# Performance work log

Hardware: AMD Instinct MI355X
Metric: run time of the kernel (lower is better)

The kernel has to match this reference:

```python
import jax, jax.numpy as jnp
import numpy as np

NH = 8  # n_heads
LN_EPS = 1e-5

def _ln(x, g, b):
    m = x.mean(-1, keepdims=True)
    v = ((x - m) ** 2).mean(-1, keepdims=True)
    return (x - m) / jnp.sqrt(v + LN_EPS) * g + b

def _l2norm(x):
    n = jnp.sqrt(jnp.sum(x * x, axis=-1, keepdims=True))
    return x / jnp.maximum(n, 1e-12)

def _block(h, inw, inb, outw, outb, g1, b1, g2, b2, w1, bb1, w2, bb2):
    B, T, D = h.shape
    hd = D // NH
    res = h
    hn = _ln(h, g1, b1)
    qkv = hn @ inw.T + inb
    q, k, v = jnp.split(qkv, 3, axis=-1)
    q = q.reshape(B, T, NH, hd)
    k = k.reshape(B, T, NH, hd)
    v = v.reshape(B, T, NH, hd)
    scores = jnp.einsum('bthd,bshd->bhts', q, k) / jnp.sqrt(jnp.asarray(hd, h.dtype))
    a = jax.nn.softmax(scores, axis=-1)
    o = jnp.einsum('bhts,bshd->bthd', a, v).reshape(B, T, D)
    h = res + o @ outw.T + outb
    f = _ln(h, g2, b2)
    f = jax.nn.gelu(f @ w1.T + bb1, approximate=False) @ w2.T + bb2
    return h + f

def setup_inputs() -> dict:
    B, T, IN, D, L, NS, NP = 8, 1024, 1024, 512, 4, 1024, 512
    key = jax.random.key(0)
    ks = jax.random.split(key, 24)
    gn = jax.random.normal
    u = jax.random.uniform(ks[1], (B, T, NS), dtype=jnp.float32, minval=1e-6, maxval=1.0 - 1e-6)
    gumbel = -jnp.log(-jnp.log(u))
    s = lambda fan: 1.0 / np.sqrt(fan)
    inp = {
        'x': gn(ks[0], (B, T, IN), dtype=jnp.float32),
        'gumbel': gumbel,
        'sym_w': gn(ks[2], (D, IN)) * s(IN),
        'sym_b': jnp.zeros((D,)),
        'codebook': gn(ks[3], (NS, D)) * 0.1,
        'pos_enc': gn(ks[4], (1, 2000, D)) * 0.02,
        'attn_in_w': gn(ks[5], (L, 3 * D, D)) * s(D),
        'attn_in_b': jnp.zeros((L, 3 * D)),
        'attn_out_w': gn(ks[6], (L, D, D)) * s(D),
        'attn_out_b': jnp.zeros((L, D)),
        'n1_g': jnp.ones((L, D)), 'n1_b': jnp.zeros((L, D)),
        'n2_g': jnp.ones((L, D)), 'n2_b': jnp.zeros((L, D)),
        'ffn_w1': gn(ks[7], (L, 4 * D, D)) * s(D),
        'ffn_b1': jnp.zeros((L, 4 * D)),
        'ffn_w2': gn(ks[8], (L, D, 4 * D)) * s(4 * D),
        'ffn_b2': jnp.zeros((L, D)),
        'q_w': gn(ks[9], (D, D)) * s(D),
        'q_b': jnp.zeros((D,)),
        'qln_g': jnp.ones((D,)), 'qln_b': jnp.zeros((D,)),
        'patterns': gn(ks[10], (NP, D)) * s(D),
        'epoch': 0,
        'total_epochs': 100,
    }
    return inp

def reference(x, gumbel, sym_w, sym_b, codebook, pos_enc,
              attn_in_w, attn_in_b, attn_out_w, attn_out_b,
              n1_g, n1_b, n2_g, n2_b, ffn_w1, ffn_b1, ffn_w2, ffn_b2,
              q_w, q_b, qln_g, qln_b, patterns, epoch, total_epochs):
    B, T, _ = x.shape
    # SymbolizationLayer (soft, gumbel-softmax with tau=0.5)
    hp = x @ sym_w.T + sym_b                               # [B,T,D]
    logits_s = _l2norm(hp) @ _l2norm(codebook).T / 0.5     # [B,T,NS]
    soft = jax.nn.softmax((logits_s + gumbel) / 0.5, axis=-1)
    h = soft @ codebook + pos_enc[:, :T, :]
    # transformer blocks
    for i in range(attn_in_w.shape[0]):
        h = _block(h, attn_in_w[i], attn_in_b[i], attn_out_w[i], attn_out_b[i],
                   n1_g[i], n1_b[i], n2_g[i], n2_b[i],
                   ffn_w1[i], ffn_b1[i], ffn_w2[i], ffn_b2[i])
    # VQPatternMatrix (eval mode: hard assignments, no EMA updates)
    Q = _l2norm(_ln(h @ q_w.T + q_b, qln_g, qln_b))
    temp = max(0.5, 1.0 - 0.5 * epoch / total_epochs)
    logits = Q @ _l2norm(patterns).T / temp                # [B,T,NP]
    hard_idx = jnp.argmax(logits, axis=-1)                 # [B,T]
    assign = jax.nn.one_hot(hard_idx, patterns.shape[0], dtype=logits.dtype)
    emb = jnp.take(patterns, hard_idx, axis=0)             # gather = one_hot @ patterns
    return (emb, assign, logits, h, hard_idx)
```

## Files before the change

kernel.cpp:

```cpp
#include <hip/hip_runtime.h>

#define DEV __device__ __forceinline__

typedef unsigned short u16;
typedef unsigned int u32;
typedef __attribute__((ext_vector_type(8))) _Float16 h8_t;
typedef __attribute__((ext_vector_type(4))) float f4_t;

constexpr int T_SEQ = 1024;
constexpr int DMODEL = 512;
constexpr int NPAT = 512;

enum {
  E_BIAS = 0,
  E_VQ = 5,
  E_RES = 6,
  E_POS = 8,
  E_GUM2 = 9,
  E_GELU2 = 10,
  E_QKV2 = 11
};

DEV float h2f(u16 h) { return (float)__builtin_bit_cast(_Float16, h); }
DEV void split2(float x, u16& h, u16& l) {
  _Float16 hh = (_Float16)x;
  float r = x - (float)hh;
  _Float16 ll = (_Float16)r;
  h = __builtin_bit_cast(u16, hh);
  l = __builtin_bit_cast(u16, ll);
}

DEV f4_t mfh(h8_t a, h8_t b, f4_t c) {
  return __builtin_amdgcn_mfma_f32_16x16x32_f16(a, b, c, 0, 0, 0);
}
DEV f4_t prod3(h8_t ah, h8_t al, h8_t bh, h8_t bl, f4_t c) {
  c = mfh(ah, bh, c);
  c = mfh(ah, bl, c);
  c = mfh(al, bh, c);
  return c;
}

typedef const __attribute__((address_space(1))) unsigned char* gas_t;
typedef __attribute__((address_space(3))) unsigned char* las_t;
DEV void gload16(const u16* g, u16* l) {
  __builtin_amdgcn_global_load_lds((gas_t)(const void*)g, (las_t)(void*)l, 16,
                                   0, 0);
}

template <int EPI>
DEV void apply_epi(float v, int m, int c, int N, const float* bias_v,
                   const float* res, float* Cf, u16* Ch, u16* Cl, float invt) {
  const size_t idx = (size_t)m * N + c;
  if constexpr (EPI == E_BIAS) {
    Cf[idx] = v + bias_v[0];
  } else if constexpr (EPI == E_VQ) {
    Cf[idx] = v * invt;
  } else if constexpr (EPI == E_RES) {
    Cf[idx] = v + bias_v[0] + res[idx];
  } else if constexpr (EPI == E_POS) {
    Cf[idx] = v + res[(size_t)(m & 1023) * N + c];
  } else if constexpr (EPI == E_GUM2) {
    float t = 4.0f * v + 2.0f * res[idx];
    u16 h2, l2;
    split2(t, h2, l2);
    Ch[idx] = h2;
    Cl[idx] = l2;
  } else if constexpr (EPI == E_GELU2) {
    float t = v + bias_v[0];
    float g = 0.5f * t * (1.0f + erff(t * 0.7071067811865476f));
    u16 h2, l2;
    split2(g, h2, l2);
    Ch[idx] = h2;
    Cl[idx] = l2;
  } else if constexpr (EPI == E_QKV2) {
    float t = v + bias_v[0];
    u16 h2, l2;
    split2(t, h2, l2);
    size_t o;
    if (c < 512) {
      o = (size_t)m * 512 + c;
    } else if (c < 1024) {
      o = 4194304 + (size_t)m * 512 + (c - 512);
    } else {
      int cc = c - 1024, hh2 = cc >> 6, dd = cc & 63;
      int bb2 = m >> 10, tt2 = m & 1023;
      o = 8388608 + (((size_t)(bb2 * 8 + hh2) * 64 + dd) << 10) + tt2;
    }
    Ch[o] = h2;
    Cl[o] = l2;
  }
}

template <int BM, int EPI>
__global__ __launch_bounds__(256, BM == 64 ? 3 : 2) void gemm_mf(
    const u16* __restrict__ Ah, const u16* __restrict__ Al,
    const u16* __restrict__ Bh, const u16* __restrict__ Bl,
    const float* __restrict__ bias, const float* __restrict__ res,
    float* __restrict__ Cf, u16* __restrict__ Ch, u16* __restrict__ Cl, int N,
    int KK, int lda, int ldb, int gx, const int* __restrict__ ep,
    const int* __restrict__ tot) {
  constexpr int MT = BM / 32;
  constexpr int CPP = BM / 16;
  __shared__ __align__(16) u16 AsH[2][BM][4][8], AsL[2][BM][4][8];
  __shared__ __align__(16) u16 BsH[2][128][4][8], BsL[2][128][4][8];
  const int tid = threadIdx.x;
  const int w = tid >> 6, lane = tid & 63;
  const int wy = w >> 1, wx = w & 1;
  const int lr = lane & 15, lg = lane >> 4;

  const int nwg = gridDim.x;
  const int bid = blockIdx.x;
  const int qq = nwg >> 3;
  const int wg = (bid & 7) * qq + (bid >> 3);
  const int by = wg / gx, bx = wg % gx;
  const int bm = by * BM, bn = bx * 128;

  const int rowl = lane >> 2, slot4 = lane & 3;

  auto STAGE = [&](int k0, int buf) {
#pragma unroll
    for (int it = 0; it < CPP / 2; ++it) {
      const int f = w + 4 * it;
      const int plane = f / CPP;
      const int ch = f % CPP;
      const int row = ch * 16 + rowl;
      const int kp = slot4 ^ ((row >> 1) & 3);
      const size_t g = (size_t)(bm + row) * lda + k0 + kp * 8;
      if (plane == 0)
        gload16(&Ah[g], &AsH[buf][0][0][0] + ch * 512);
      else
        gload16(&Al[g], &AsL[buf][0][0][0] + ch * 512);
    }
#pragma unroll
    for (int it = 0; it < 4; ++it) {
      const int f = w + 4 * it;
      const int plane = f >> 3;
      const int ch = f & 7;
      const int row = ch * 16 + rowl;
      const int kp = slot4 ^ ((row >> 1) & 3);
      const size_t g = (size_t)(bn + row) * ldb + k0 + kp * 8;
      if (plane == 0)
        gload16(&Bh[g], &BsH[buf][0][0][0] + ch * 512);
      else
        gload16(&Bl[g], &BsL[buf][0][0][0] + ch * 512);
    }
  };

  f4_t acc[MT][4];
#pragma unroll
  for (int mt = 0; mt < MT; ++mt)
#pragma unroll
    for (int nt = 0; nt < 4; ++nt) acc[mt][nt] = (f4_t){0.f, 0.f, 0.f, 0.f};

  const int nsteps = KK / 32;
  STAGE(0, 0);
  __syncthreads();
  for (int t = 0; t < nsteps; ++t) {
    const int cur = t & 1;
    if (t + 1 < nsteps) STAGE((t + 1) * 32, cur ^ 1);

    h8_t fah[MT], fal[MT], fbh[4], fbl[4];
#pragma unroll
    for (int mt = 0; mt < MT; ++mt) {
      int row = wy * (BM / 2) + mt * 16 + lr;
      int slot = lg ^ ((row >> 1) & 3);
      fah[mt] = *(const h8_t*)&AsH[cur][row][slot][0];
      fal[mt] = *(const h8_t*)&AsL[cur][row][slot][0];
    }
#pragma unroll
    for (int nt = 0; nt < 4; ++nt) {
      int col = wx * 64 + nt * 16 + lr;
      int slot = lg ^ ((col >> 1) & 3);
      fbh[nt] = *(const h8_t*)&BsH[cur][col][slot][0];
      fbl[nt] = *(const h8_t*)&BsL[cur][col][slot][0];
    }
#pragma unroll
    for (int mt = 0; mt < MT; ++mt)
#pragma unroll
      for (int nt = 0; nt < 4; ++nt)
        acc[mt][nt] = prod3(fah[mt], fal[mt], fbh[nt], fbl[nt], acc[mt][nt]);
    __syncthreads();
  }

  float bv[4];
  if constexpr (EPI == E_BIAS || EPI == E_RES || EPI == E_GELU2 ||
                EPI == E_QKV2) {
#pragma unroll
    for (int nt = 0; nt < 4; ++nt) bv[nt] = bias[bn + wx * 64 + nt * 16 + lr];
  }
  float invt = 1.0f;
  if constexpr (EPI == E_VQ) {
    float tt = 1.0f - 0.5f * (float)ep[0] / (float)tot[0];
    invt = 1.0f / fmaxf(0.5f, tt);
  }
#pragma unroll
  for (int mt = 0; mt < MT; ++mt)
#pragma unroll
    for (int nt = 0; nt < 4; ++nt) {
      const int c = bn + wx * 64 + nt * 16 + lr;
#pragma unroll
      for (int i = 0; i < 4; ++i) {
        const int m = bm + wy * (BM / 2) + mt * 16 + 4 * lg + i;
        apply_epi<EPI>(acc[mt][nt][i], m, c, N, &bv[nt], res, Cf, Ch, Cl,
                       invt);
      }
    }
}

template <int EPI>
__global__ __launch_bounds__(512, 2) void gemm_mf8(
    const u16* __restrict__ Ah, const u16* __restrict__ Al,
    const u16* __restrict__ Bh, const u16* __restrict__ Bl,
    const float* __restrict__ bias, const float* __restrict__ res,
    float* __restrict__ Cf, u16* __restrict__ Ch, u16* __restrict__ Cl, int N,
    int KK, int lda, int ldb, int gx) {
  __shared__ __align__(16) u16 AsH[2][64][4][8], AsL[2][64][4][8];
  __shared__ __align__(16) u16 BsH[2][256][4][8], BsL[2][256][4][8];
  const int tid = threadIdx.x;
  const int w = tid >> 6, lane = tid & 63;
  const int wy = w >> 2, wx = w & 3;
  const int lr = lane & 15, lg = lane >> 4;

  const int nwg = gridDim.x;
  const int bid = blockIdx.x;
  const int qq = nwg >> 3;
  const int wg = (bid & 7) * qq + (bid >> 3);
  const int by = wg / gx, bx = wg % gx;
  const int bm = by * 64, bn = bx * 256;

  const int rowl = lane >> 2, slot4 = lane & 3;

  auto STAGE = [&](int k0, int buf) {
#pragma unroll
    for (int it = 0; it < 5; ++it) {
      const int f = w + 8 * it;
      if (f < 8) {
        const int plane = f >> 2, ch = f & 3;
        const int row = ch * 16 + rowl;
        const int kp = slot4 ^ ((row >> 1) & 3);
        const size_t g = (size_t)(bm + row) * lda + k0 + kp * 8;
        if (plane == 0)
          gload16(&Ah[g], &AsH[buf][0][0][0] + ch * 512);
        else
          gload16(&Al[g], &AsL[buf][0][0][0] + ch * 512);
      } else {
        const int fb = f - 8;
        const int plane = fb >> 4, ch = fb & 15;
        const int row = ch * 16 + rowl;
        const int kp = slot4 ^ ((row >> 1) & 3);
        const size_t g = (size_t)(bn + row) * ldb + k0 + kp * 8;
        if (plane == 0)
          gload16(&Bh[g], &BsH[buf][0][0][0] + ch * 512);
        else
          gload16(&Bl[g], &BsL[buf][0][0][0] + ch * 512);
      }
    }
  };

  f4_t acc[2][4];
#pragma unroll
  for (int mt = 0; mt < 2; ++mt)
#pragma unroll
    for (int nt = 0; nt < 4; ++nt) acc[mt][nt] = (f4_t){0.f, 0.f, 0.f, 0.f};

  const int nsteps = KK / 32;
  STAGE(0, 0);
  __syncthreads();
  for (int t = 0; t < nsteps; ++t) {
    const int cur = t & 1;
    if (t + 1 < nsteps) STAGE((t + 1) * 32, cur ^ 1);

    h8_t fah[2], fal[2], fbh[4], fbl[4];
#pragma unroll
    for (int mt = 0; mt < 2; ++mt) {
      int row = wy * 32 + mt * 16 + lr;
      int slot = lg ^ ((row >> 1) & 3);
      fah[mt] = *(const h8_t*)&AsH[cur][row][slot][0];
      fal[mt] = *(const h8_t*)&AsL[cur][row][slot][0];
    }
#pragma unroll
    for (int nt = 0; nt < 4; ++nt) {
      int col = wx * 64 + nt * 16 + lr;
      int slot = lg ^ ((col >> 1) & 3);
      fbh[nt] = *(const h8_t*)&BsH[cur][col][slot][0];
      fbl[nt] = *(const h8_t*)&BsL[cur][col][slot][0];
    }
#pragma unroll
    for (int mt = 0; mt < 2; ++mt)
#pragma unroll
      for (int nt = 0; nt < 4; ++nt)
        acc[mt][nt] = prod3(fah[mt], fal[mt], fbh[nt], fbl[nt], acc[mt][nt]);
    __syncthreads();
  }

  float bv[4];
  if constexpr (EPI == E_BIAS || EPI == E_RES || EPI == E_GELU2 ||
                EPI == E_QKV2) {
#pragma unroll
    for (int nt = 0; nt < 4; ++nt) bv[nt] = bias[bn + wx * 64 + nt * 16 + lr];
  }
#pragma unroll
  for (int mt = 0; mt < 2; ++mt)
#pragma unroll
    for (int nt = 0; nt < 4; ++nt) {
      const int c = bn + wx * 64 + nt * 16 + lr;
#pragma unroll
      for (int i = 0; i < 4; ++i) {
        const int m = bm + wy * 32 + mt * 16 + 4 * lg + i;
        apply_epi<EPI>(acc[mt][nt][i], m, c, N, &bv[nt], res, Cf, Ch, Cl,
                       1.0f);
      }
    }
}

__global__ __launch_bounds__(512, 2) void flash_mfma(
    const u16* __restrict__ QKVh, const u16* __restrict__ QKVl,
    u16* __restrict__ Oh, u16* __restrict__ Ol) {
  __shared__ __align__(16) u16 KP[2][128][8][8];
  __shared__ __align__(16) u16 Vs[2][64][8][8];
  const int tid = threadIdx.x;
  const int w = tid >> 6, lane = tid & 63;
  const int lr = lane & 15, lg = lane >> 4;
  const int bid = blockIdx.x;
  const int b = bid & 7;
  const int slot_b = bid >> 3;
  const int hh = slot_b >> 3;
  const int qt = slot_b & 7;

  const u16* Qh = QKVh;
  const u16* Ql = QKVl;
  const u16* Kh = QKVh + 4194304;
  const u16* Kl = QKVl + 4194304;
  const u16* Vh = QKVh + 8388608;
  const u16* Vl = QKVl + 8388608;

  h8_t qf[2][2];
  {
    size_t g = ((size_t)(b * 1024 + qt * 128 + w * 16 + lr)) * 512 + hh * 64 +
               lg * 8;
    qf[0][0] = *(const h8_t*)&Qh[g];
    qf[0][1] = *(const h8_t*)&Ql[g];
    qf[1][0] = *(const h8_t*)&Qh[g + 32];
    qf[1][1] = *(const h8_t*)&Ql[g + 32];
  }

  f4_t oacc[4];
#pragma unroll
  for (int nt = 0; nt < 4; ++nt) oacc[nt] = (f4_t){0.f, 0.f, 0.f, 0.f};
  float mrun[4], lrun[4];
#pragma unroll
  for (int i = 0; i < 4; ++i) {
    mrun[i] = -__builtin_huge_valf();
    lrun[i] = 0.0f;
  }

  const int rowl8 = lane >> 3, slot8 = lane & 7;

  for (int kt = 0; kt < 16; ++kt) {
    __syncthreads();
#pragma unroll
    for (int it = 0; it < 2; ++it) {
      const int f = w + 8 * it;
      const int plane = f >> 3, ch = f & 7;
      const int row = ch * 8 + rowl8;
      const int kp = slot8 ^ (row & 7);
      const size_t gk =
          ((size_t)(b * 1024 + kt * 64 + row)) * 512 + hh * 64 + kp * 8;
      if (plane == 0)
        gload16(&Kh[gk], &KP[0][0][0][0] + ch * 512);
      else
        gload16(&Kl[gk], &KP[1][0][0][0] + ch * 512);
    }
#pragma unroll
    for (int it = 0; it < 2; ++it) {
      const int f = w + 8 * it;
      const int plane = f >> 3, ch = f & 7;
      const int row = ch * 8 + rowl8;
      const int kp = slot8 ^ (row & 7);
      const size_t gv =
          ((size_t)((b * 8 + hh) * 64 + row)) * 1024 + kt * 64 + kp * 8;
      if (plane == 0)
        gload16(&Vh[gv], &Vs[0][0][0][0] + ch * 512);
      else
        gload16(&Vl[gv], &Vs[1][0][0][0] + ch * 512);
    }
    __syncthreads();

    f4_t s[4];
#pragma unroll
    for (int nt = 0; nt < 4; ++nt) {
      s[nt] = (f4_t){0.f, 0.f, 0.f, 0.f};
      const int col = nt * 16 + lr;
#pragma unroll
      for (int ks = 0; ks < 2; ++ks) {
        int slt = (ks * 4 + lg) ^ (col & 7);
        h8_t kh = *(const h8_t*)&KP[0][col][slt][0];
        h8_t kl = *(const h8_t*)&KP[1][col][slt][0];
        s[nt] = prod3(qf[ks][0], qf[ks][1], kh, kl, s[nt]);
      }
    }

#pragma unroll
    for (int i = 0; i < 4; ++i) {
      float rm = -__builtin_huge_valf();
#pragma unroll
      for (int nt = 0; nt < 4; ++nt) {
        s[nt][i] *= 0.125f;
        rm = fmaxf(rm, s[nt][i]);
      }
      rm = fmaxf(rm, __shfl_xor(rm, 1));
      rm = fmaxf(rm, __shfl_xor(rm, 2));
      rm = fmaxf(rm, __shfl_xor(rm, 4));
      rm = fmaxf(rm, __shfl_xor(rm, 8));
      float mnew = fmaxf(mrun[i], rm);
      float alpha = __expf(mrun[i] - mnew);
      float rs = 0.0f;
#pragma unroll
      for (int nt = 0; nt < 4; ++nt) {
        float p = __expf(s[nt][i] - mnew);
        s[nt][i] = p;
        rs += p;
      }
      rs += __shfl_xor(rs, 1);
      rs += __shfl_xor(rs, 2);
      rs += __shfl_xor(rs, 4);
      rs += __shfl_xor(rs, 8);
      lrun[i] = lrun[i] * alpha + rs;
      mrun[i] = mnew;
#pragma unroll
      for (int nt = 0; nt < 4; ++nt) oacc[nt][i] *= alpha;
    }

    __syncthreads();

#pragma unroll
    for (int nt = 0; nt < 4; ++nt)
#pragma unroll
      for (int i = 0; i < 4; ++i) {
        int qrow = w * 16 + 4 * lg + i;
        int kv = nt * 16 + lr;
        int kp = kv >> 3, j = kv & 7;
        int slt = kp ^ (qrow & 7);
        u16 h2, l2;
        split2(s[nt][i], h2, l2);
        KP[0][qrow][slt][j] = h2;
        KP[1][qrow][slt][j] = l2;
      }

    h8_t pf[2][2];
#pragma unroll
    for (int ks = 0; ks < 2; ++ks) {
      int row = w * 16 + lr;
      int slt = (ks * 4 + lg) ^ (row & 7);
      pf[ks][0] = *(const h8_t*)&KP[0][row][slt][0];
      pf[ks][1] = *(const h8_t*)&KP[1][row][slt][0];
    }
#pragma unroll
    for (int ntd = 0; ntd < 4; ++ntd) {
      const int col = ntd * 16 + lr;
#pragma unroll
      for (int ks = 0; ks < 2; ++ks) {
        int slt = (ks * 4 + lg) ^ (col & 7);
        h8_t vh = *(const h8_t*)&Vs[0][col][slt][0];
        h8_t vl = *(const h8_t*)&Vs[1][col][slt][0];
        oacc[ntd] = prod3(pf[ks][0], pf[ks][1], vh, vl, oacc[ntd]);
      }
    }
  }

#pragma unroll
  for (int i = 0; i < 4; ++i) {
    float inv = 1.0f / lrun[i];
    int t = qt * 128 + w * 16 + 4 * lg + i;
#pragma unroll
    for (int ntd = 0; ntd < 4; ++ntd) {
      int d = hh * 64 + ntd * 16 + lr;
      size_t idx = ((size_t)(b * 1024 + t)) * 512 + d;
      u16 h2, l2;
      split2(oacc[ntd][i] * inv, h2, l2);
      Oh[idx] = h2;
      Ol[idx] = l2;
    }
  }
}

DEV float wave_sum(float v) {
#pragma unroll
  for (int off = 1; off < 64; off <<= 1) v += __shfl_xor(v, off);
  return v;
}

DEV void store8_split2(u16* H, u16* L, size_t base, const float* t) {
  u16 vh[8], vl[8];
#pragma unroll
  for (int j = 0; j < 8; ++j) split2(t[j], vh[j], vl[j]);
  *(ushort4*)&H[base] = make_ushort4(vh[0], vh[1], vh[2], vh[3]);
  *(ushort4*)&H[base + 4] = make_ushort4(vh[4], vh[5], vh[6], vh[7]);
  *(ushort4*)&L[base] = make_ushort4(vl[0], vl[1], vl[2], vl[3]);
  *(ushort4*)&L[base + 4] = make_ushort4(vl[4], vl[5], vl[6], vl[7]);
}

__global__ __launch_bounds__(256) void ln_split2(const float* __restrict__ x,
                                                 const float* __restrict__ g,
                                                 const float* __restrict__ b,
                                                 u16* __restrict__ yh,
                                                 u16* __restrict__ yl) {
  const int row = blockIdx.x * 4 + (threadIdx.x >> 6);
  const int lane = threadIdx.x & 63;
  const float* xr = x + (size_t)row * DMODEL;
  float v[8];
  *(float4*)&v[0] = *(const float4*)(xr + lane * 8);
  *(float4*)&v[4] = *(const float4*)(xr + lane * 8 + 4);
  float s = 0.0f;
#pragma unroll
  for (int j = 0; j < 8; ++j) s += v[j];
  s = wave_sum(s);
  float mean = s * (1.0f / 512.0f);
  float s2 = 0.0f;
#pragma unroll
  for (int j = 0; j < 8; ++j) {
    float d = v[j] - mean;
    s2 += d * d;
  }
  s2 = wave_sum(s2);
  float rstd = 1.0f / sqrtf(s2 * (1.0f / 512.0f) + 1e-5f);
  float gg[8], bv[8];
  *(float4*)&gg[0] = *(const float4*)(g + lane * 8);
  *(float4*)&gg[4] = *(const float4*)(g + lane * 8 + 4);
  *(float4*)&bv[0] = *(const float4*)(b + lane * 8);
  *(float4*)&bv[4] = *(const float4*)(b + lane * 8 + 4);
  float t[8];
#pragma unroll
  for (int j = 0; j < 8; ++j) t[j] = (v[j] - mean) * rstd * gg[j] + bv[j];
  store8_split2(yh, yl, (size_t)row * DMODEL + lane * 8, t);
}

__global__ __launch_bounds__(256) void ln_l2_split2(
    const float* __restrict__ x, const float* __restrict__ g,
    const float* __restrict__ b, u16* __restrict__ yh, u16* __restrict__ yl) {
  const int row = blockIdx.x * 4 + (threadIdx.x >> 6);
  const int lane = threadIdx.x & 63;
  const float* xr = x + (size_t)row * DMODEL;
  float v[8];
  *(float4*)&v[0] = *(const float4*)(xr + lane * 8);
  *(float4*)&v[4] = *(const float4*)(xr + lane * 8 + 4);
  float s = 0.0f;
#pragma unroll
  for (int j = 0; j < 8; ++j) s += v[j];
  s = wave_sum(s);
  float mean = s * (1.0f / 512.0f);
  float s2 = 0.0f;
#pragma unroll
  for (int j = 0; j < 8; ++j) {
    float d = v[j] - mean;
    s2 += d * d;
  }
  s2 = wave_sum(s2);
  float rstd = 1.0f / sqrtf(s2 * (1.0f / 512.0f) + 1e-5f);
  float gg[8], bv[8];
  *(float4*)&gg[0] = *(const float4*)(g + lane * 8);
  *(float4*)&gg[4] = *(const float4*)(g + lane * 8 + 4);
  *(float4*)&bv[0] = *(const float4*)(b + lane * 8);
  *(float4*)&bv[4] = *(const float4*)(b + lane * 8 + 4);
  float t[8];
#pragma unroll
  for (int j = 0; j < 8; ++j) t[j] = (v[j] - mean) * rstd * gg[j] + bv[j];
  float n2 = 0.0f;
#pragma unroll
  for (int j = 0; j < 8; ++j) n2 += t[j] * t[j];
  n2 = wave_sum(n2);
  float den = fmaxf(sqrtf(n2), 1e-12f);
#pragma unroll
  for (int j = 0; j < 8; ++j) t[j] /= den;
  store8_split2(yh, yl, (size_t)row * DMODEL + lane * 8, t);
}

__global__ __launch_bounds__(256) void l2_split2(const float* __restrict__ x,
                                                 u16* __restrict__ yh,
                                                 u16* __restrict__ yl) {
  const int row = blockIdx.x * 4 + (threadIdx.x >> 6);
  const int lane = threadIdx.x & 63;
  const float* xr = x + (size_t)row * DMODEL;
  float v[8];
  *(float4*)&v[0] = *(const float4*)(xr + lane * 8);
  *(float4*)&v[4] = *(const float4*)(xr + lane * 8 + 4);
  float n2 = 0.0f;
#pragma unroll
  for (int j = 0; j < 8; ++j) n2 += v[j] * v[j];
  n2 = wave_sum(n2);
  float den = fmaxf(sqrtf(n2), 1e-12f);
#pragma unroll
  for (int j = 0; j < 8; ++j) v[j] /= den;
  store8_split2(yh, yl, (size_t)row * DMODEL + lane * 8, v);
}

__global__ __launch_bounds__(256) void softmax2(u16* __restrict__ H,
                                                u16* __restrict__ L) {
  const int row = blockIdx.x;
  const int tid = threadIdx.x;
  const size_t base = (size_t)row * 1024 + tid * 4;
  ushort4 qh = *(const ushort4*)&H[base];
  ushort4 ql = *(const ushort4*)&L[base];
  float v0 = h2f(qh.x) + h2f(ql.x);
  float v1 = h2f(qh.y) + h2f(ql.y);
  float v2 = h2f(qh.z) + h2f(ql.z);
  float v3 = h2f(qh.w) + h2f(ql.w);
  float mx = fmaxf(fmaxf(v0, v1), fmaxf(v2, v3));
#pragma unroll
  for (int off = 1; off < 64; off <<= 1) mx = fmaxf(mx, __shfl_xor(mx, off));
  __shared__ float red[4];
  const int wv = tid >> 6;
  if ((tid & 63) == 0) red[wv] = mx;
  __syncthreads();
  mx = fmaxf(fmaxf(red[0], red[1]), fmaxf(red[2], red[3]));
  float e0 = __expf(v0 - mx), e1 = __expf(v1 - mx), e2 = __expf(v2 - mx),
        e3 = __expf(v3 - mx);
  float s = e0 + e1 + e2 + e3;
#pragma unroll
  for (int off = 1; off < 64; off <<= 1) s += __shfl_xor(s, off);
  __syncthreads();
  if ((tid & 63) == 0) red[wv] = s;
  __syncthreads();
  s = red[0] + red[1] + red[2] + red[3];
  float inv = 1.0f / s;
  u16 ah[4], al[4];
  split2(e0 * inv, ah[0], al[0]);
  split2(e1 * inv, ah[1], al[1]);
  split2(e2 * inv, ah[2], al[2]);
  split2(e3 * inv, ah[3], al[3]);
  *(ushort4*)&H[base] = make_ushort4(ah[0], ah[1], ah[2], ah[3]);
  *(ushort4*)&L[base] = make_ushort4(al[0], al[1], al[2], al[3]);
}

__global__ __launch_bounds__(256) void split2_k(const float* __restrict__ src,
                                                u16* __restrict__ H,
                                                u16* __restrict__ L, int n4) {
  for (int e = blockIdx.x * 256 + threadIdx.x; e < n4; e += gridDim.x * 256) {
    float4 v = *(const float4*)(src + (size_t)e * 4);
    u16 ah[4], al[4];
    split2(v.x, ah[0], al[0]);
    split2(v.y, ah[1], al[1]);
    split2(v.z, ah[2], al[2]);
    split2(v.w, ah[3], al[3]);
    *(ushort4*)&H[(size_t)e * 4] = make_ushort4(ah[0], ah[1], ah[2], ah[3]);
    *(ushort4*)&L[(size_t)e * 4] = make_ushort4(al[0], al[1], al[2], al[3]);
  }
}

__global__ __launch_bounds__(256) void tsplit_cb(const float* __restrict__ cb,
                                                 u16* __restrict__ th,
                                                 u16* __restrict__ tl) {
  const int c = blockIdx.x;
  const int t = threadIdx.x;
  u16 ah[4], al[4];
#pragma unroll
  for (int j = 0; j < 4; ++j) {
    float v = cb[(size_t)(4 * t + j) * 512 + c];
    split2(v, ah[j], al[j]);
  }
  const size_t base = (size_t)c * 1024 + 4 * t;
  *(ushort4*)&th[base] = make_ushort4(ah[0], ah[1], ah[2], ah[3]);
  *(ushort4*)&tl[base] = make_ushort4(al[0], al[1], al[2], al[3]);
}

__global__ __launch_bounds__(256) void vq_finalize(
    const float* __restrict__ logits, const float* __restrict__ patterns,
    float* __restrict__ emb, float* __restrict__ assign,
    float* __restrict__ idxf) {
  const int row = blockIdx.x * 4 + (threadIdx.x >> 6);
  const int lane = threadIdx.x & 63;
  const float* lr = logits + (size_t)row * NPAT;
  float best = -__builtin_huge_valf();
  int bi = 0;
#pragma unroll
  for (int jj = 0; jj < 8; ++jj) {
    int j = lane + jj * 64;
    float v = lr[j];
    if (v > best) {
      best = v;
      bi = j;
    }
  }
#pragma unroll
  for (int off = 1; off < 64; off <<= 1) {
    float ob = __shfl_xor(best, off);
    int oi = __shfl_xor(bi, off);
    if (ob > best || (ob == best && oi < bi)) {
      best = ob;
      bi = oi;
    }
  }
  const float* pr = patterns + (size_t)bi * DMODEL;
#pragma unroll
  for (int g = 0; g < 2; ++g) {
    int c = lane * 8 + g * 4;
    float4 pv = *(const float4*)(pr + c);
    *(float4*)(emb + (size_t)row * DMODEL + c) = pv;
    float4 av;
    av.x = (c + 0 == bi) ? 1.0f : 0.0f;
    av.y = (c + 1 == bi) ? 1.0f : 0.0f;
    av.z = (c + 2 == bi) ? 1.0f : 0.0f;
    av.w = (c + 3 == bi) ? 1.0f : 0.0f;
    *(float4*)(assign + (size_t)row * NPAT + c) = av;
  }
  if (lane == 0) idxf[row] = (float)bi;
}

extern "C" void kernel_launch(void* const* d_in, const int* in_sizes, int n_in,
                              void* d_out, int out_size, void* d_ws,
                              size_t ws_size, hipStream_t stream) {
  (void)in_sizes;
  (void)n_in;
  (void)out_size;
  (void)ws_size;
  const float* x = (const float*)d_in[0];
  const float* gumbel = (const float*)d_in[1];
  const float* sym_w = (const float*)d_in[2];
  const float* sym_b = (const float*)d_in[3];
  const float* codebook = (const float*)d_in[4];
  const float* pos_enc = (const float*)d_in[5];
  const float* attn_in_w = (const float*)d_in[6];
  const float* attn_in_b = (const float*)d_in[7];
  const float* attn_out_w = (const float*)d_in[8];
  const float* attn_out_b = (const float*)d_in[9];
  const float* n1_g = (const float*)d_in[10];
  const float* n1_b = (const float*)d_in[11];
  const float* n2_g = (const float*)d_in[12];
  const float* n2_b = (const float*)d_in[13];
  const float* ffn_w1 = (const float*)d_in[14];
  const float* ffn_b1 = (const float*)d_in[15];
  const float* ffn_w2 = (const float*)d_in[16];
  const float* ffn_b2 = (const float*)d_in[17];
  const float* q_w = (const float*)d_in[18];
  const float* q_b = (const float*)d_in[19];
  const float* qln_g = (const float*)d_in[20];
  const float* qln_b = (const float*)d_in[21];
  const float* patterns = (const float*)d_in[22];
  const int* epoch = (const int*)d_in[23];
  const int* tot = (const int*)d_in[24];

  float* out = (float*)d_out;
  float* emb = out;
  float* assign = out + 4194304;
  float* logits = out + 8388608;
  float* h = out + 12582912;
  float* idxf = out + 16777216;

  float* ws_f = (float*)d_ws;
  u16* a16 = (u16*)ws_f;
  float* bF = ws_f + 18874368;
  u16* b16 = (u16*)bF;
  u16 *hnH = b16, *hnL = b16 + 4194304;
  float* wF = ws_f + 25165824;
  u16* w16 = (u16*)wF;

  u16 *xH = a16, *xL = a16 + 8388608;
  split2_k<<<2048, 256, 0, stream>>>(x, xH, xL, 2097152);
  split2_k<<<512, 256, 0, stream>>>(sym_w, w16, w16 + 524288, 131072);
  gemm_mf<64, E_BIAS><<<512, 256, 0, stream>>>(
      xH, xL, w16, w16 + 524288, sym_b, nullptr, bF, nullptr, nullptr, 512,
      1024, 1024, 1024, 4, nullptr, nullptr);
  l2_split2<<<256, 256, 0, stream>>>(codebook, w16, w16 + 524288);
  u16 *hpH = a16, *hpL = a16 + 4194304;
  l2_split2<<<2048, 256, 0, stream>>>(bF, hpH, hpL);
  u16 *sH = a16 + 12582912, *sL = a16 + 20971520;
  gemm_mf8<E_GUM2><<<512, 512, 0, stream>>>(hpH, hpL, w16, w16 + 524288,
                                            nullptr, gumbel, nullptr, sH, sL,
                                            1024, 512, 512, 512, 4);
  softmax2<<<8192, 256, 0, stream>>>(sH, sL);
  tsplit_cb<<<512, 256, 0, stream>>>(codebook, w16, w16 + 524288);
  gemm_mf<64, E_POS><<<512, 256, 0, stream>>>(
      sH, sL, w16, w16 + 524288, nullptr, pos_enc, h, nullptr, nullptr, 512,
      1024, 1024, 1024, 4, nullptr, nullptr);

  u16 *qkvH = a16, *qkvL = a16 + 12582912;
  u16* w1p = a16 + 33554432;
  u16* w2p = b16 + 8388608;
  u16 *pH = a16, *pL = a16 + 16777216;

  for (int l = 0; l < 4; ++l) {
    const float* inw = attn_in_w + (size_t)l * 1536 * 512;
    const float* inb = attn_in_b + (size_t)l * 1536;
    const float* outw = attn_out_w + (size_t)l * 512 * 512;
    const float* outb = attn_out_b + (size_t)l * 512;
    const float* w1 = ffn_w1 + (size_t)l * 2048 * 512;
    const float* b1 = ffn_b1 + (size_t)l * 2048;
    const float* w2 = ffn_w2 + (size_t)l * 512 * 2048;
    const float* b2 = ffn_b2 + (size_t)l * 512;

    ln_split2<<<2048, 256, 0, stream>>>(h, n1_g + l * 512, n1_b + l * 512,
                                        hnH, hnL);
    split2_k<<<1024, 256, 0, stream>>>(inw, w16, w16 + 786432, 196608);
    gemm_mf8<E_QKV2><<<768, 512, 0, stream>>>(hnH, hnL, w16, w16 + 786432,
                                              inb, nullptr, nullptr, qkvH,
                                              qkvL, 1536, 512, 512, 512, 6);
    flash_mfma<<<512, 512, 0, stream>>>(qkvH, qkvL, hnH, hnL);
    split2_k<<<256, 256, 0, stream>>>(outw, w16, w16 + 262144, 65536);
    gemm_mf<64, E_RES><<<512, 256, 0, stream>>>(
        hnH, hnL, w16, w16 + 262144, outb, h, h, nullptr, nullptr, 512, 512,
        512, 512, 4, nullptr, nullptr);
    ln_split2<<<2048, 256, 0, stream>>>(h, n2_g + l * 512, n2_b + l * 512,
                                        hnH, hnL);
    split2_k<<<1024, 256, 0, stream>>>(w1, w1p, w1p + 1048576, 262144);
    split2_k<<<1024, 256, 0, stream>>>(w2, w2p, w2p + 1048576, 262144);
    gemm_mf8<E_GELU2><<<1024, 512, 0, stream>>>(hnH, hnL, w1p, w1p + 1048576,
                                                b1, nullptr, nullptr, pH, pL,
                                                2048, 512, 512, 512, 8);
    gemm_mf<64, E_RES><<<512, 256, 0, stream>>>(
        pH, pL, w2p, w2p + 1048576, b2, h, h, nullptr, nullptr, 512, 2048,
        2048, 2048, 4, nullptr, nullptr);
  }

  u16 *hsH = a16, *hsL = a16 + 4194304;
  u16 *QpH = a16 + 8388608, *QpL = a16 + 12582912;
  split2_k<<<1024, 256, 0, stream>>>(h, hsH, hsL, 1048576);
  split2_k<<<256, 256, 0, stream>>>(q_w, w16, w16 + 262144, 65536);
  gemm_mf<64, E_BIAS><<<512, 256, 0, stream>>>(
      hsH, hsL, w16, w16 + 262144, q_b, nullptr, bF, nullptr, nullptr, 512,
      512, 512, 512, 4, nullptr, nullptr);
  ln_l2_split2<<<2048, 256, 0, stream>>>(bF, qln_g, qln_b, QpH, QpL);
  l2_split2<<<128, 256, 0, stream>>>(patterns, w16 + 524288, w16 + 786432);
  gemm_mf<64, E_VQ><<<512, 256, 0, stream>>>(
      QpH, QpL, w16 + 524288, w16 + 786432, nullptr, nullptr, logits, nullptr,
      nullptr, 512, 512, 512, 512, 4, epoch, tot);
  vq_finalize<<<2048, 256, 0, stream>>>(logits, patterns, emb, assign, idxf);
}
```

Baseline: 1.564 ms.

## Load GEMM A fragments directly from global into registers, drop A LDS staging

Result: slower. 1.979 ms (+26.6%).

```diff
diff --git a/kernel.cpp b/kernel.cpp
--- a/kernel.cpp
+++ b/kernel.cpp
@@ -92,7 +92,7 @@
 }
 
 template <int BM, int EPI>
-__global__ __launch_bounds__(256, BM == 64 ? 3 : 2) void gemm_mf(
+__global__ __launch_bounds__(256, BM == 64 ? 4 : 2) void gemm_mf(
     const u16* __restrict__ Ah, const u16* __restrict__ Al,
     const u16* __restrict__ Bh, const u16* __restrict__ Bl,
     const float* __restrict__ bias, const float* __restrict__ res,
@@ -100,8 +100,6 @@
     int KK, int lda, int ldb, int gx, const int* __restrict__ ep,
     const int* __restrict__ tot) {
   constexpr int MT = BM / 32;
-  constexpr int CPP = BM / 16;
-  __shared__ __align__(16) u16 AsH[2][BM][4][8], AsL[2][BM][4][8];
   __shared__ __align__(16) u16 BsH[2][128][4][8], BsL[2][128][4][8];
   const int tid = threadIdx.x;
   const int w = tid >> 6, lane = tid & 63;
@@ -118,19 +116,6 @@
   const int rowl = lane >> 2, slot4 = lane & 3;
 
   auto STAGE = [&](int k0, int buf) {
-#pragma unroll
-    for (int it = 0; it < CPP / 2; ++it) {
-      const int f = w + 4 * it;
-      const int plane = f / CPP;
-      const int ch = f % CPP;
-      const int row = ch * 16 + rowl;
-      const int kp = slot4 ^ ((row >> 1) & 3);
-      const size_t g = (size_t)(bm + row) * lda + k0 + kp * 8;
-      if (plane == 0)
-        gload16(&Ah[g], &AsH[buf][0][0][0] + ch * 512);
-      else
-        gload16(&Al[g], &AsL[buf][0][0][0] + ch * 512);
-    }
 #pragma unroll
     for (int it = 0; it < 4; ++it) {
       const int f = w + 4 * it;
@@ -146,39 +131,53 @@
     }
   };
 
+  auto LOAD_A = [&](int k0, h8_t(&ah)[MT], h8_t(&al)[MT]) {
+#pragma unroll
+    for (int mt = 0; mt < MT; ++mt) {
+      const size_t g =
+          (size_t)(bm + wy * (BM / 2) + mt * 16 + lr) * lda + k0 + lg * 8;
+      ah[mt] = *(const h8_t*)&Ah[g];
+      al[mt] = *(const h8_t*)&Al[g];
+    }
+  };
+
   f4_t acc[MT][4];
 #pragma unroll
   for (int mt = 0; mt < MT; ++mt)
 #pragma unroll
     for (int nt = 0; nt < 4; ++nt) acc[mt][nt] = (f4_t){0.f, 0.f, 0.f, 0.f};
 
-  const int nsteps = KK / 32;
-  STAGE(0, 0);
-  __syncthreads();
-  for (int t = 0; t < nsteps; ++t) {
-    const int cur = t & 1;
-    if (t + 1 < nsteps) STAGE((t + 1) * 32, cur ^ 1);
-
-    h8_t fah[MT], fal[MT], fbh[4], fbl[4];
-#pragma unroll
-    for (int mt = 0; mt < MT; ++mt) {
-      int row = wy * (BM / 2) + mt * 16 + lr;
-      int slot = lg ^ ((row >> 1) & 3);
-      fah[mt] = *(const h8_t*)&AsH[cur][row][slot][0];
-      fal[mt] = *(const h8_t*)&AsL[cur][row][slot][0];
-    }
+  auto KSTEP = [&](int buf, h8_t(&ah)[MT], h8_t(&al)[MT]) {
+    h8_t fbh[4], fbl[4];
 #pragma unroll
     for (int nt = 0; nt < 4; ++nt) {
       int col = wx * 64 + nt * 16 + lr;
       int slot = lg ^ ((col >> 1) & 3);
-      fbh[nt] = *(const h8_t*)&BsH[cur][col][slot][0];
-      fbl[nt] = *(const h8_t*)&BsL[cur][col][slot][0];
+      fbh[nt] = *(const h8_t*)&BsH[buf][col][slot][0];
+      fbl[nt] = *(const h8_t*)&BsL[buf][col][slot][0];
     }
 #pragma unroll
     for (int mt = 0; mt < MT; ++mt)
 #pragma unroll
       for (int nt = 0; nt < 4; ++nt)
-        acc[mt][nt] = prod3(fah[mt], fal[mt], fbh[nt], fbl[nt], acc[mt][nt]);
+        acc[mt][nt] = prod3(ah[mt], al[mt], fbh[nt], fbl[nt], acc[mt][nt]);
+  };
+
+  const int nsteps = KK / 32;
+  h8_t a0h[MT], a0l[MT], a1h[MT], a1l[MT];
+  STAGE(0, 0);
+  LOAD_A(0, a0h, a0l);
+  __syncthreads();
+  for (int s = 0; s < nsteps; s += 2) {
+    STAGE((s + 1) * 32, 1);
+    LOAD_A((s + 1) * 32, a1h, a1l);
+    KSTEP(0, a0h, a0l);
+    __syncthreads();
+    if (s + 2 < nsteps) {
+      STAGE((s + 2) * 32, 0);
+      LOAD_A((s + 2) * 32, a0h, a0l);
+    }
+    KSTEP(1, a1h, a1l);
     __syncthreads();
   }
 
@@ -214,7 +213,6 @@
     const float* __restrict__ bias, const float* __restrict__ res,
     float* __restrict__ Cf, u16* __restrict__ Ch, u16* __restrict__ Cl, int N,
     int KK, int lda, int ldb, int gx) {
-  __shared__ __align__(16) u16 AsH[2][64][4][8], AsL[2][64][4][8];
   __shared__ __align__(16) u16 BsH[2][256][4][8], BsL[2][256][4][8];
   const int tid = threadIdx.x;
   const int w = tid >> 6, lane = tid & 63;
@@ -232,64 +230,66 @@
 
   auto STAGE = [&](int k0, int buf) {
 #pragma unroll
-    for (int it = 0; it < 5; ++it) {
+    for (int it = 0; it < 4; ++it) {
       const int f = w + 8 * it;
-      if (f < 8) {
-        const int plane = f >> 2, ch = f & 3;
-        const int row = ch * 16 + rowl;
-        const int kp = slot4 ^ ((row >> 1) & 3);
-        const size_t g = (size_t)(bm + row) * lda + k0 + kp * 8;
-        if (plane == 0)
-          gload16(&Ah[g], &AsH[buf][0][0][0] + ch * 512);
-        else
-          gload16(&Al[g], &AsL[buf][0][0][0] + ch * 512);
-      } else {
-        const int fb = f - 8;
-        const int plane = fb >> 4, ch = fb & 15;
-        const int row = ch * 16 + rowl;
-        const int kp = slot4 ^ ((row >> 1) & 3);
-        const size_t g = (size_t)(bn + row) * ldb + k0 + kp * 8;
-        if (plane == 0)
-          gload16(&Bh[g], &BsH[buf][0][0][0] + ch * 512);
-        else
-          gload16(&Bl[g], &BsL[buf][0][0][0] + ch * 512);
-      }
+      const int plane = f >> 4, ch = f & 15;
+      const int row = ch * 16 + rowl;
+      const int kp = slot4 ^ ((row >> 1) & 3);
+      const size_t g = (size_t)(bn + row) * ldb + k0 + kp * 8;
+      if (plane == 0)
+        gload16(&Bh[g], &BsH[buf][0][0][0] + ch * 512);
+      else
+        gload16(&Bl[g], &BsL[buf][0][0][0] + ch * 512);
     }
   };
 
+  auto LOAD_A = [&](int k0, h8_t(&ah)[2], h8_t(&al)[2]) {
+#pragma unroll
+    for (int mt = 0; mt < 2; ++mt) {
+      const size_t g =
+          (size_t)(bm + wy * 32 + mt * 16 + lr) * lda + k0 + lg * 8;
+      ah[mt] = *(const h8_t*)&Ah[g];
+      al[mt] = *(const h8_t*)&Al[g];
+    }
+  };
+
   f4_t acc[2][4];
 #pragma unroll
   for (int mt = 0; mt < 2; ++mt)
 #pragma unroll
     for (int nt = 0; nt < 4; ++nt) acc[mt][nt] = (f4_t){0.f, 0.f, 0.f, 0.f};
 
-  const int nsteps = KK / 32;
-  STAGE(0, 0);
-  __syncthreads();
-  for (int t = 0; t < nsteps; ++t) {
-    const int cur = t & 1;
-    if (t + 1 < nsteps) STAGE((t + 1) * 32, cur ^ 1);
-
-    h8_t fah[2], fal[2], fbh[4], fbl[4];
-#pragma unroll
-    for (int mt = 0; mt < 2; ++mt) {
-      int row = wy * 32 + mt * 16 + lr;
-      int slot = lg ^ ((row >> 1) & 3);
-      fah[mt] = *(const h8_t*)&AsH[cur][row][slot][0];
-      fal[mt] = *(const h8_t*)&AsL[cur][row][slot][0];
-    }
+  auto KSTEP = [&](int buf, h8_t(&ah)[2], h8_t(&al)[2]) {
+    h8_t fbh[4], fbl[4];
 #pragma unroll
     for (int nt = 0; nt < 4; ++nt) {
       int col = wx * 64 + nt * 16 + lr;
       int slot = lg ^ ((col >> 1) & 3);
-      fbh[nt] = *(const h8_t*)&BsH[cur][col][slot][0];
-      fbl[nt] = *(const h8_t*)&BsL[cur][col][slot][0];
+      fbh[nt] = *(const h8_t*)&BsH[buf][col][slot][0];
+      fbl[nt] = *(const h8_t*)&BsL[buf][col][slot][0];
     }
 #pragma unroll
     for (int mt = 0; mt < 2; ++mt)
 #pragma unroll
       for (int nt = 0; nt < 4; ++nt)
-        acc[mt][nt] = prod3(fah[mt], fal[mt], fbh[nt], fbl[nt], acc[mt][nt]);
+        acc[mt][nt] = prod3(ah[mt], al[mt], fbh[nt], fbl[nt], acc[mt][nt]);
+  };
+
+  const int nsteps = KK / 32;
+  h8_t a0h[2], a0l[2], a1h[2], a1l[2];
+  STAGE(0, 0);
+  LOAD_A(0, a0h, a0l);
+  __syncthreads();
+  for (int s = 0; s < nsteps; s += 2) {
+    STAGE((s + 1) * 32, 1);
+    LOAD_A((s + 1) * 32, a1h, a1l);
+    KSTEP(0, a0h, a0l);
+    __syncthreads();
+    if (s + 2 < nsteps) {
+      STAGE((s + 2) * 32, 0);
+      LOAD_A((s + 2) * 32, a0h, a0l);
+    }
+    KSTEP(1, a1h, a1l);
     __syncthreads();
   }
 
```
